# Optimization experiments

Measured on AMD Instinct MI355X. Metric: run time of the kernel, lower is better.

The kernel has to match this reference:

```python
import jax, jax.numpy as jnp
import numpy as np

L, B, E, H, NH = 128, 32, 128, 256, 8
NUM_NODE, ETA = 20000, 100


def setup_inputs() -> dict:
    key = jax.random.key(0)
    ks = jax.random.split(key, 24)
    s = 0.05
    rn = lambda k, sh: jax.random.normal(k, sh, dtype=jnp.float32) * s
    return {
        "node": jax.random.randint(ks[0], (L, B), 0, NUM_NODE + 1),
        "ts": jax.random.normal(ks[1], (L, B, 2), dtype=jnp.float32),
        "seq_lengths": jnp.sort(jax.random.randint(ks[2], (B,), 64, L + 1))[::-1],
        "embed_table": rn(ks[3], (NUM_NODE + 1, E)),
        "Wih0": rn(ks[4], (3 * H, E + 2)), "Whh0": rn(ks[5], (3 * H, H)),
        "bih0": rn(ks[6], (3 * H,)), "bhh0": rn(ks[7], (3 * H,)),
        "Wih1": rn(ks[8], (3 * H, H)), "Whh1": rn(ks[9], (3 * H, H)),
        "bih1": rn(ks[10], (3 * H,)), "bhh1": rn(ks[11], (3 * H,)),
        "Wa0": rn(ks[12], (E, 2 * E)), "ba0": rn(ks[13], (E,)),
        "Wa1": rn(ks[14], (NH, E)), "ba1": rn(ks[15], (NH,)),
        "Wf0": rn(ks[16], (168, H * (NH + 1))), "bf0": rn(ks[17], (168,)),
        "Wf1": rn(ks[18], (ETA, 168)), "bf1": rn(ks[19], (ETA,)),
    }


def gru_layer(x, Wih, Whh, bih, bhh, lengths):
    # x: [L, B, in]; PyTorch GRU cell, with pack/pad semantics:
    # hidden frozen and output zeroed for t >= length (emulates pack_padded_sequence).
    Lx, Bx, _ = x.shape

    def step(h, xs):
        x_t, t = xs
        gi = x_t @ Wih.T + bih          # [B, 3H]
        gh = h @ Whh.T + bhh            # [B, 3H]
        ir, iz, in_ = jnp.split(gi, 3, axis=-1)
        hr, hz, hn = jnp.split(gh, 3, axis=-1)
        r = jax.nn.sigmoid(ir + hr)
        z = jax.nn.sigmoid(iz + hz)
        n = jnp.tanh(in_ + r * hn)
        h_new = (1.0 - z) * n + z * h
        valid = (t < lengths)[:, None]
        h = jnp.where(valid, h_new, h)
        return h, jnp.where(valid, h_new, jnp.zeros_like(h_new))

    h0 = jnp.zeros((Bx, Whh.shape[1]), x.dtype)
    hT, outs = jax.lax.scan(step, h0, (x, jnp.arange(Lx)))
    return outs, hT


def reference(node, ts, seq_lengths, embed_table,
              Wih0, Whh0, bih0, bhh0, Wih1, Whh1, bih1, bhh1,
              Wa0, ba0, Wa1, ba1, Wf0, bf0, Wf1, bf1):
    e = embed_table[node]                          # [L, B, E]
    embeds = jnp.concatenate([e, ts], axis=-1)     # [L, B, E+2]

    # pairwise attention: a[i,j] = e[j], b[i,j] = e[i] (repeat + transpose)
    a = jnp.broadcast_to(e[None], (L, L, B, E))
    b = jnp.broadcast_to(e[:, None], (L, L, B, E))
    pair = jnp.concatenate([a, b], axis=-1)        # [L, L, B, 2E]
    hid = jax.nn.relu(pair @ Wa0.T + ba0)          # [L, L, B, E]
    w = (hid @ Wa1.T + ba1).sum(axis=1)            # [L, B, NH]

    # multiplicative length mask, then softmax over time axis (as in original)
    mask = (jnp.arange(L)[:, None] < seq_lengths[None, :]).astype(w.dtype)[..., None]
    w = jax.nn.softmax(w * mask, axis=0)           # [L, B, NH]

    out0, _ = gru_layer(embeds, Wih0, Whh0, bih0, bhh0, seq_lengths)
    out1, hT = gru_layer(out0, Wih1, Whh1, bih1, bhh1, seq_lengths)  # [L,B,H], [B,H]

    ctx = jnp.einsum('lbh,lbd->bhd', w, out1).reshape(B, NH * H)     # [B, NH*H]
    z = jnp.concatenate([ctx, hT], axis=-1) @ Wf0.T + bf0
    z = jax.nn.selu(z)
    logits = z @ Wf1.T + bf1
    return jax.nn.log_softmax(logits, axis=-1)
```

## Files before the change

kernel.cpp:

```cpp
#include <hip/hip_runtime.h>
#include <hip/hip_bf16.h>

#define LL 128
#define BB 32
#define EE 128
#define HH 256
#define NHH 8
#define G3 768
#define IN0 130
#define ETA 100
#define F1 168
#define CLSIN 2304

typedef _Float16 half_t;
typedef __attribute__((ext_vector_type(2))) _Float16 half2v;
typedef __attribute__((ext_vector_type(8))) _Float16 f16x8;
typedef __attribute__((ext_vector_type(4))) float f32x4;

#if defined(__has_builtin)
#if __has_builtin(__builtin_amdgcn_fdot2)
#define HAVE_FDOT2 1
#endif
#endif

__device__ __forceinline__ float fdot2f(half2v a, half2v b, float c) {
#ifdef HAVE_FDOT2
  return __builtin_amdgcn_fdot2(a, b, c, false);
#else
  return c + (float)a.x * (float)b.x + (float)a.y * (float)b.y;
#endif
}

#define BARRIER_LDS() __asm__ volatile("s_waitcnt lgkmcnt(0)\n\ts_barrier" ::: "memory")

__device__ __forceinline__ float sigmoidf_(float x) { return 1.0f / (1.0f + __expf(-x)); }
__device__ __forceinline__ float tanhf_(float x) { return 1.0f - 2.0f / (__expf(2.0f * x) + 1.0f); }

__global__ void prep_kernel(
    const float* __restrict__ Wa0, const float* __restrict__ Wih0,
    const float* __restrict__ Wih1, const float* __restrict__ Whh0,
    const float* __restrict__ Whh1,
    half_t* __restrict__ Wa0Ta, half_t* __restrict__ Wa0Tb,
    half2v* __restrict__ Wih0T2, half2v* __restrict__ Wih1T2,
    half_t* __restrict__ Whh0h, half_t* __restrict__ Whh1h)
{
  int idx = blockIdx.x * blockDim.x + threadIdx.x;
  const int n1 = 16384, n2 = 16384, n3 = 65 * 768, n4 = 128 * 768, n5 = 196608;
  if (idx < n1) {
    int d = idx >> 7, k = idx & 127;
    Wa0Ta[idx] = (half_t)Wa0[k * 256 + d];
  } else if ((idx -= n1) < n2) {
    int d = idx >> 7, k = idx & 127;
    Wa0Tb[idx] = (half_t)Wa0[k * 256 + 128 + d];
  } else if ((idx -= n2) < n3) {
    int d2 = idx / 768, r = idx % 768;
    half2v w; w.x = (half_t)Wih0[r * IN0 + 2 * d2]; w.y = (half_t)Wih0[r * IN0 + 2 * d2 + 1];
    Wih0T2[idx] = w;
  } else if ((idx -= n3) < n4) {
    int d2 = idx / 768, r = idx % 768;
    half2v w; w.x = (half_t)Wih1[r * HH + 2 * d2]; w.y = (half_t)Wih1[r * HH + 2 * d2 + 1];
    Wih1T2[idx] = w;
  } else if ((idx -= n4) < n5) {
    Whh0h[idx] = (half_t)Whh0[idx];
  } else if ((idx -= n5) < n5) {
    Whh1h[idx] = (half_t)Whh1[idx];
  }
}

__global__ void embed_uv_kernel(
    const int* __restrict__ node,
    const float* __restrict__ table,
    const half_t* __restrict__ Wa0Ta,
    const half_t* __restrict__ Wa0Tb,
    const float* __restrict__ ba0,
    half2v* __restrict__ e_h2,
    float* __restrict__ U,
    float* __restrict__ V)
{
  int lb = blockIdx.x;
  int k = threadIdx.x;
  __shared__ float es[EE];
  int n = node[lb];
  float ev = table[(size_t)n * EE + k];
  es[k] = ev;
  __syncthreads();
  if (k < 64) {
    half2v p; p.x = (half_t)es[2 * k]; p.y = (half_t)es[2 * k + 1];
    e_h2[(size_t)lb * 64 + k] = p;
  }
  float u = 0.f, v = ba0[k];
  #pragma unroll 8
  for (int d = 0; d < EE; ++d) {
    float x = es[d];
    u += (float)Wa0Ta[d * EE + k] * x;
    v += (float)Wa0Tb[d * EE + k] * x;
  }
  U[(size_t)lb * EE + k] = u;
  V[(size_t)lb * EE + k] = v;
}

__global__ __launch_bounds__(128) void attn_w_kernel(
    const float* __restrict__ U, const float* __restrict__ V,
    const float* __restrict__ Wa1,
    const float* __restrict__ ba1,
    float* __restrict__ wpre)
{
  int ig = blockIdx.x >> 5;
  int b = blockIdx.x & 31;
  int i0 = ig * 4;
  int k = threadIdx.x;
  float vk[4];
  #pragma unroll
  for (int ii = 0; ii < 4; ++ii) vk[ii] = V[((size_t)(i0 + ii) * BB + b) * EE + k];
  float wa[NHH], acc[4][NHH];
  #pragma unroll
  for (int h = 0; h < NHH; ++h) wa[h] = Wa1[h * EE + k];
  #pragma unroll
  for (int ii = 0; ii < 4; ++ii)
    #pragma unroll
    for (int h = 0; h < NHH; ++h) acc[ii][h] = 0.f;
  for (int j = 0; j < LL; ++j) {
    float u = U[((size_t)j * BB + b) * EE + k];
    #pragma unroll
    for (int ii = 0; ii < 4; ++ii) {
      float tv = fmaxf(u + vk[ii], 0.f);
      #pragma unroll
      for (int h = 0; h < NHH; ++h) acc[ii][h] += wa[h] * tv;
    }
  }
  __shared__ float part[2][32];
  int wave = k >> 6, lane = k & 63;
  #pragma unroll
  for (int ii = 0; ii < 4; ++ii)
    #pragma unroll
    for (int h = 0; h < NHH; ++h) {
      float a = acc[ii][h];
      #pragma unroll
      for (int off = 32; off > 0; off >>= 1) a += __shfl_xor(a, off, 64);
      if (lane == 0) part[wave][ii * 8 + h] = a;
    }
  __syncthreads();
  if (k < 32) {
    int ii = k >> 3, h = k & 7;
    float w = part[0][k] + part[1][k] + (float)LL * ba1[h];
    wpre[((size_t)(i0 + ii) * BB + b) * NHH + h] = w;
  }
}

__global__ void attn_softmax_kernel(
    const float* __restrict__ wpre, const int* __restrict__ slen,
    float* __restrict__ wsoft)
{
  int b = blockIdx.x >> 3;
  int h = blockIdx.x & 7;
  int l = threadIdx.x;
  int len = slen[b];
  float x = wpre[((size_t)l * BB + b) * NHH + h];
  float xv = (l < len) ? x : 0.f;
  float m = xv;
  #pragma unroll
  for (int off = 32; off > 0; off >>= 1) m = fmaxf(m, __shfl_xor(m, off, 64));
  __shared__ float sm[2], ss[2];
  int wave = l >> 6;
  if ((l & 63) == 0) sm[wave] = m;
  __syncthreads();
  m = fmaxf(sm[0], sm[1]);
  float e = __expf(xv - m);
  float s = e;
  #pragma unroll
  for (int off = 32; off > 0; off >>= 1) s += __shfl_xor(s, off, 64);
  if ((l & 63) == 0) ss[wave] = s;
  __syncthreads();
  s = ss[0] + ss[1];
  wsoft[((size_t)l * BB + b) * NHH + h] = e / s;
}

__global__ __launch_bounds__(256) void gi0_kernel(
    const half2v* __restrict__ e_h2, const float* __restrict__ ts,
    const half2v* __restrict__ W2,
    const float* __restrict__ bih,
    float* __restrict__ gi)
{
  int lb0 = blockIdx.x * 8;
  int tid = threadIdx.x;
  __shared__ half2v xs2[8][66];
  for (int idx = tid; idx < 512; idx += 256) {
    int q = idx >> 6, d2 = idx & 63;
    xs2[q][d2] = e_h2[(size_t)(lb0 + q) * 64 + d2];
  }
  if (tid < 8) {
    half2v t2; t2.x = (half_t)ts[(lb0 + tid) * 2]; t2.y = (half_t)ts[(lb0 + tid) * 2 + 1];
    xs2[tid][64] = t2;
  }
  __syncthreads();
  float acc[8][3];
  #pragma unroll
  for (int q = 0; q < 8; ++q) { acc[q][0] = 0.f; acc[q][1] = 0.f; acc[q][2] = 0.f; }
  for (int d2 = 0; d2 < 65; ++d2) {
    half2v w0 = W2[d2 * 768 + tid];
    half2v w1 = W2[d2 * 768 + 256 + tid];
    half2v w2 = W2[d2 * 768 + 512 + tid];
    #pragma unroll
    for (int q = 0; q < 8; ++q) {
      half2v x = xs2[q][d2];
      acc[q][0] = fdot2f(w0, x, acc[q][0]);
      acc[q][1] = fdot2f(w1, x, acc[q][1]);
      acc[q][2] = fdot2f(w2, x, acc[q][2]);
    }
  }
  float b0 = bih[tid], b1 = bih[256 + tid], b2 = bih[512 + tid];
  #pragma unroll
  for (int q = 0; q < 8; ++q) {
    float* gp = gi + (size_t)(lb0 + q) * G3;
    gp[tid] = acc[q][0] + b0; gp[256 + tid] = acc[q][1] + b1; gp[512 + tid] = acc[q][2] + b2;
  }
}

__global__ __launch_bounds__(256) void gi1_kernel(
    const float* __restrict__ out0,
    const half2v* __restrict__ W2,
    const float* __restrict__ bih,
    float* __restrict__ gi)
{
  int lb0 = blockIdx.x * 8;
  int tid = threadIdx.x;
  __shared__ half2v xs2[8][128];
  for (int idx = tid; idx < 1024; idx += 256) {
    int q = idx >> 7, d2 = idx & 127;
    float2 v = ((const float2*)(out0 + (size_t)(lb0 + q) * HH))[d2];
    half2v x; x.x = (half_t)v.x; x.y = (half_t)v.y;
    xs2[q][d2] = x;
  }
  __syncthreads();
  float acc[8][3];
  #pragma unroll
  for (int q = 0; q < 8; ++q) { acc[q][0] = 0.f; acc[q][1] = 0.f; acc[q][2] = 0.f; }
  for (int d2 = 0; d2 < 128; ++d2) {
    half2v w0 = W2[d2 * 768 + tid];
    half2v w1 = W2[d2 * 768 + 256 + tid];
    half2v w2 = W2[d2 * 768 + 512 + tid];
    #pragma unroll
    for (int q = 0; q < 8; ++q) {
      half2v x = xs2[q][d2];
      acc[q][0] = fdot2f(w0, x, acc[q][0]);
      acc[q][1] = fdot2f(w1, x, acc[q][1]);
      acc[q][2] = fdot2f(w2, x, acc[q][2]);
    }
  }
  float b0 = bih[tid], b1 = bih[256 + tid], b2 = bih[512 + tid];
  #pragma unroll
  for (int q = 0; q < 8; ++q) {
    float* gp = gi + (size_t)(lb0 + q) * G3;
    gp[tid] = acc[q][0] + b0; gp[256 + tid] = acc[q][1] + b1; gp[512 + tid] = acc[q][2] + b2;
  }
}

__global__ __launch_bounds__(512, 2) void gru_scan_kernel(
    const half_t* __restrict__ Whhh,
    const float* __restrict__ bhh,
    const float* __restrict__ gi,
    const int* __restrict__ slen,
    float* __restrict__ out,
    float* __restrict__ hT)
{
  const int b = blockIdx.x;
  const int tid = threadIdx.x;
  const int w = tid >> 6;
  const int lane = tid & 63;
  const int m = lane & 15;
  const int kg = lane >> 4;

  __shared__ __align__(16) half_t hshared[HH];
  __shared__ __align__(16) float gsum[G3];

  f16x8 A[48];
  {
    const half_t* wbase = Whhh + (size_t)(w * 96 + m) * HH + kg * 8;
    #pragma unroll
    for (int tl = 0; tl < 6; ++tl)
      #pragma unroll
      for (int kc = 0; kc < 8; ++kc)
        A[tl * 8 + kc] = *(const f16x8*)(wbase + (size_t)(tl * 16) * HH + kc * 32);
  }

  const int len = slen[b];
  float bhr = 0.f, bhz = 0.f, bhn = 0.f, hold = 0.f;
  if (tid < HH) {
    bhr = bhh[tid]; bhz = bhh[HH + tid]; bhn = bhh[2 * HH + tid];
    hshared[tid] = (half_t)0.f;
  }
  __syncthreads();

  const float* gib = gi + (size_t)b * G3;
  float* outb = out + (size_t)b * HH;

  #pragma unroll 1
  for (int t = 0; t < LL; ++t) {
    float g0 = 0.f, g1 = 0.f, g2 = 0.f;
    if (tid < HH) {
      const float* gp = gib + (size_t)t * (BB * G3);
      g0 = gp[tid]; g1 = gp[HH + tid]; g2 = gp[2 * HH + tid];
    }
    f32x4 C[6];
    #pragma unroll
    for (int tl = 0; tl < 6; ++tl) C[tl] = (f32x4){0.f, 0.f, 0.f, 0.f};
    #pragma unroll
    for (int kc = 0; kc < 8; ++kc) {
      f16x8 bf = *(const f16x8*)&hshared[kc * 32 + kg * 8];
      #pragma unroll
      for (int tl = 0; tl < 6; ++tl)
        C[tl] = __builtin_amdgcn_mfma_f32_16x16x32_f16(A[tl * 8 + kc], bf, C[tl], 0, 0, 0);
    }
    if (m == 0) {
      #pragma unroll
      for (int tl = 0; tl < 6; ++tl)
        *(f32x4*)&gsum[w * 96 + tl * 16 + kg * 4] = C[tl];
    }
    BARRIER_LDS();
    if (tid < HH) {
      float r_ = sigmoidf_(g0 + gsum[tid] + bhr);
      float z_ = sigmoidf_(g1 + gsum[HH + tid] + bhz);
      float n_ = tanhf_(g2 + r_ * (gsum[2 * HH + tid] + bhn));
      float hnew = (1.f - z_) * n_ + z_ * hold;
      bool valid = t < len;
      hold = valid ? hnew : hold;
      hshared[tid] = (half_t)hold;
      outb[(size_t)t * (BB * HH) + tid] = valid ? hnew : 0.f;
    }
    BARRIER_LDS();
  }
  if (tid < HH) hT[(size_t)b * HH + tid] = hold;
}

__global__ void ctx_kernel(
    const float* __restrict__ wsoft, const float* __restrict__ out1,
    float* __restrict__ ctx)
{
  int b = blockIdx.x >> 3, h = blockIdx.x & 7;
  int d = threadIdx.x;
  float acc = 0.f;
  for (int l = 0; l < LL; ++l) {
    float w = wsoft[((size_t)l * BB + b) * NHH + h];
    acc += w * out1[((size_t)l * BB + b) * HH + d];
  }
  ctx[(size_t)b * (NHH * HH) + h * HH + d] = acc;
}

__global__ __launch_bounds__(512) void final_kernel(
    const float* __restrict__ ctx, const float* __restrict__ hT,
    const float* __restrict__ Wf0,
    const float* __restrict__ bf0,
    const float* __restrict__ Wf1,
    const float* __restrict__ bf1,
    float* __restrict__ outp)
{
  int b = blockIdx.x;
  int tid = threadIdx.x;
  int wave = tid >> 6, lane = tid & 63;
  __shared__ float4 xs4[CLSIN / 4];
  __shared__ float zs[F1];
  __shared__ float ls[ETA];
  float* xs = (float*)xs4;
  for (int i = tid; i < NHH * HH; i += 512) xs[i] = ctx[(size_t)b * (NHH * HH) + i];
  if (tid < HH) xs[NHH * HH + tid] = hT[(size_t)b * HH + tid];
  __syncthreads();
  for (int r = wave; r < F1; r += 8) {
    const float4* wp = (const float4*)(Wf0 + (size_t)r * CLSIN);
    float acc = 0.f;
    #pragma unroll
    for (int i = 0; i < CLSIN / 4 / 64; ++i) {
      float4 w = wp[lane + 64 * i];
      float4 x = xs4[lane + 64 * i];
      acc += w.x * x.x + w.y * x.y + w.z * x.z + w.w * x.w;
    }
    #pragma unroll
    for (int off = 32; off > 0; off >>= 1) acc += __shfl_xor(acc, off, 64);
    if (lane == 0) {
      float x = acc + bf0[r];
      const float alpha = 1.6732632423543772f, scale = 1.0507009873554805f;
      zs[r] = scale * (x > 0.f ? x : alpha * (__expf(x) - 1.f));
    }
  }
  __syncthreads();
  for (int r = wave; r < ETA; r += 8) {
    float acc = 0.f;
    for (int k = lane; k < F1; k += 64) acc += Wf1[r * F1 + k] * zs[k];
    #pragma unroll
    for (int off = 32; off > 0; off >>= 1) acc += __shfl_xor(acc, off, 64);
    if (lane == 0) ls[r] = acc + bf1[r];
  }
  __syncthreads();
  if (wave == 0) {
    float v0 = (lane < ETA) ? ls[lane] : -1e30f;
    float v1 = (lane + 64 < ETA) ? ls[lane + 64] : -1e30f;
    float m = fmaxf(v0, v1);
    #pragma unroll
    for (int off = 32; off > 0; off >>= 1) m = fmaxf(m, __shfl_xor(m, off, 64));
    float s = __expf(v0 - m) + __expf(v1 - m);
    #pragma unroll
    for (int off = 32; off > 0; off >>= 1) s += __shfl_xor(s, off, 64);
    float lse = m + __logf(s);
    if (lane < ETA) outp[(size_t)b * ETA + lane] = v0 - lse;
    if (lane + 64 < ETA) outp[(size_t)b * ETA + lane + 64] = v1 - lse;
  }
}

extern "C" void kernel_launch(void* const* d_in, const int* in_sizes, int n_in,
                              void* d_out, int out_size, void* d_ws, size_t ws_size,
                              hipStream_t stream) {
  const int*   node  = (const int*)d_in[0];
  const float* ts    = (const float*)d_in[1];
  const int*   slen  = (const int*)d_in[2];
  const float* table = (const float*)d_in[3];
  const float* Wih0  = (const float*)d_in[4];
  const float* Whh0  = (const float*)d_in[5];
  const float* bih0  = (const float*)d_in[6];
  const float* bhh0  = (const float*)d_in[7];
  const float* Wih1  = (const float*)d_in[8];
  const float* Whh1  = (const float*)d_in[9];
  const float* bih1  = (const float*)d_in[10];
  const float* bhh1  = (const float*)d_in[11];
  const float* Wa0   = (const float*)d_in[12];
  const float* ba0   = (const float*)d_in[13];
  const float* Wa1   = (const float*)d_in[14];
  const float* ba1   = (const float*)d_in[15];
  const float* Wf0   = (const float*)d_in[16];
  const float* bf0   = (const float*)d_in[17];
  const float* Wf1   = (const float*)d_in[18];
  const float* bf1   = (const float*)d_in[19];

  char* ws = (char*)d_ws;
  size_t off = 0;
  auto alloc = [&](size_t n) { void* p = (void*)(ws + off); off += (n + 255) & ~(size_t)255; return p; };

  half2v* e_h2 = (half2v*)alloc((size_t)LL * BB * 64 * 4);
  float* U     = (float*)alloc((size_t)LL * BB * EE * 4);
  float* V     = (float*)alloc((size_t)LL * BB * EE * 4);
  float* gi    = (float*)alloc((size_t)LL * BB * G3 * 4);
  float* out0  = (float*)alloc((size_t)LL * BB * HH * 4);
  float* out1  = (float*)alloc((size_t)LL * BB * HH * 4);
  float* hTb   = (float*)alloc((size_t)BB * HH * 4);
  float* wpre  = (float*)alloc((size_t)LL * BB * NHH * 4);
  float* wsoft = (float*)alloc((size_t)LL * BB * NHH * 4);
  float* ctxb  = (float*)alloc((size_t)BB * NHH * HH * 4);
  half_t* Wa0Ta = (half_t*)alloc((size_t)128 * 128 * 2);
  half_t* Wa0Tb = (half_t*)alloc((size_t)128 * 128 * 2);
  half2v* Wih0T2 = (half2v*)alloc((size_t)65 * 768 * 4);
  half2v* Wih1T2 = (half2v*)alloc((size_t)128 * 768 * 4);
  half_t* Whh0h = (half_t*)alloc((size_t)G3 * HH * 2);
  half_t* Whh1h = (half_t*)alloc((size_t)G3 * HH * 2);
  if (off > ws_size) return;

  const int prep_total = 16384 + 16384 + 65 * 768 + 128 * 768 + 196608 + 196608;
  prep_kernel<<<(prep_total + 255) / 256, 256, 0, stream>>>(
      Wa0, Wih0, Wih1, Whh0, Whh1, Wa0Ta, Wa0Tb, Wih0T2, Wih1T2, Whh0h, Whh1h);
  embed_uv_kernel<<<LL * BB, 128, 0, stream>>>(node, table, Wa0Ta, Wa0Tb, ba0, e_h2, U, V);
  attn_w_kernel<<<(LL / 4) * BB, 128, 0, stream>>>(U, V, Wa1, ba1, wpre);
  attn_softmax_kernel<<<BB * NHH, 128, 0, stream>>>(wpre, slen, wsoft);
  gi0_kernel<<<LL * BB / 8, 256, 0, stream>>>(e_h2, ts, Wih0T2, bih0, gi);
  gru_scan_kernel<<<BB, 512, 0, stream>>>(Whh0h, bhh0, gi, slen, out0, hTb);
  gi1_kernel<<<LL * BB / 8, 256, 0, stream>>>(out0, Wih1T2, bih1, gi);
  gru_scan_kernel<<<BB, 512, 0, stream>>>(Whh1h, bhh1, gi, slen, out1, hTb);
  ctx_kernel<<<BB * NHH, 256, 0, stream>>>(wsoft, out1, ctxb);
  final_kernel<<<BB, 512, 0, stream>>>(ctxb, hTb, Wf0, bf0, Wf1, bf1, (float*)d_out);
}
```

Measured before the change: 638.3 us.

## Remap GRU weight rows so each wave owns gates and double-buffer hidden state

Each wave's MFMA tiles now cover matching r, z and n rows for the same 32 hidden units. The gate nonlinearities are therefore computed directly from the accumulator registers, with no round trip through shared memory. The hidden state is double-buffered in LDS, so each timestep needs one barrier instead of two. The gi loads are vectorized and issued before the MFMAs. The cost is more registers per thread and gate math repeated across lanes that share the same output.

```diff
diff --git a/kernel.cpp b/kernel.cpp
--- a/kernel.cpp
+++ b/kernel.cpp
@@ -14,6 +14,7 @@
 
 typedef _Float16 half_t;
 typedef __attribute__((ext_vector_type(2))) _Float16 half2v;
+typedef __attribute__((ext_vector_type(4))) _Float16 half4v;
 typedef __attribute__((ext_vector_type(8))) _Float16 f16x8;
 typedef __attribute__((ext_vector_type(4))) float f32x4;
 
@@ -270,25 +271,29 @@
   const int m = lane & 15;
   const int kg = lane >> 4;
 
-  __shared__ __align__(16) half_t hshared[HH];
-  __shared__ __align__(16) float gsum[G3];
+  __shared__ __align__(16) half_t hbuf[2][HH];
 
   f16x8 A[48];
-  {
-    const half_t* wbase = Whhh + (size_t)(w * 96 + m) * HH + kg * 8;
-    #pragma unroll
-    for (int tl = 0; tl < 6; ++tl)
-      #pragma unroll
-      for (int kc = 0; kc < 8; ++kc)
-        A[tl * 8 + kc] = *(const f16x8*)(wbase + (size_t)(tl * 16) * HH + kc * 32);
+  #pragma unroll
+  for (int tl = 0; tl < 6; ++tl) {
+    int row = ((tl >> 1) << 8) + w * 32 + ((tl & 1) << 4) + m;
+    const half_t* wbase = Whhh + (size_t)row * HH + kg * 8;
+    #pragma unroll
+    for (int kc = 0; kc < 8; ++kc)
+      A[tl * 8 + kc] = *(const f16x8*)(wbase + kc * 32);
   }
 
   const int len = slen[b];
-  float bhr = 0.f, bhz = 0.f, bhn = 0.f, hold = 0.f;
-  if (tid < HH) {
-    bhr = bhh[tid]; bhz = bhh[HH + tid]; bhn = bhh[2 * HH + tid];
-    hshared[tid] = (half_t)0.f;
-  }
+  const int u0 = w * 32 + kg * 4;
+  float4 br[2], bz[2], bn[2];
+  #pragma unroll
+  for (int j = 0; j < 2; ++j) {
+    br[j] = *(const float4*)(bhh + u0 + j * 16);
+    bz[j] = *(const float4*)(bhh + HH + u0 + j * 16);
+    bn[j] = *(const float4*)(bhh + 2 * HH + u0 + j * 16);
+  }
+  float hold[2][4] = {{0.f, 0.f, 0.f, 0.f}, {0.f, 0.f, 0.f, 0.f}};
+  if (tid < HH) { hbuf[0][tid] = (half_t)0.f; hbuf[1][tid] = (half_t)0.f; }
   __syncthreads();
 
   const float* gib = gi + (size_t)b * G3;
@@ -296,40 +301,64 @@
 
   #pragma unroll 1
   for (int t = 0; t < LL; ++t) {
-    float g0 = 0.f, g1 = 0.f, g2 = 0.f;
-    if (tid < HH) {
-      const float* gp = gib + (size_t)t * (BB * G3);
-      g0 = gp[tid]; g1 = gp[HH + tid]; g2 = gp[2 * HH + tid];
-    }
+    const int p = t & 1;
+    const float* gp = gib + (size_t)t * (BB * G3);
+    float4 gr[2], gz[2], gn[2];
+    #pragma unroll
+    for (int j = 0; j < 2; ++j) {
+      gr[j] = *(const float4*)(gp + u0 + j * 16);
+      gz[j] = *(const float4*)(gp + HH + u0 + j * 16);
+      gn[j] = *(const float4*)(gp + 2 * HH + u0 + j * 16);
+    }
+    f16x8 bf[8];
+    #pragma unroll
+    for (int kc = 0; kc < 8; ++kc)
+      bf[kc] = *(const f16x8*)&hbuf[p][kc * 32 + kg * 8];
     f32x4 C[6];
     #pragma unroll
     for (int tl = 0; tl < 6; ++tl) C[tl] = (f32x4){0.f, 0.f, 0.f, 0.f};
     #pragma unroll
-    for (int kc = 0; kc < 8; ++kc) {
-      f16x8 bf = *(const f16x8*)&hshared[kc * 32 + kg * 8];
+    for (int kc = 0; kc < 8; ++kc)
       #pragma unroll
       for (int tl = 0; tl < 6; ++tl)
-        C[tl] = __builtin_amdgcn_mfma_f32_16x16x32_f16(A[tl * 8 + kc], bf, C[tl], 0, 0, 0);
-    }
-    if (m == 0) {
+        C[tl] = __builtin_amdgcn_mfma_f32_16x16x32_f16(A[tl * 8 + kc], bf[kc], C[tl], 0, 0, 0);
+    bool valid = t < len;
+    #pragma unroll
+    for (int j = 0; j < 2; ++j) {
+      float4 ov;
+      half4v hv;
       #pragma unroll
-      for (int tl = 0; tl < 6; ++tl)
-        *(f32x4*)&gsum[w * 96 + tl * 16 + kg * 4] = C[tl];
+      for (int reg = 0; reg < 4; ++reg) {
+        float grv = (reg == 0 ? gr[j].x : reg == 1 ? gr[j].y : reg == 2 ? gr[j].z : gr[j].w);
+        float gzv = (reg == 0 ? gz[j].x : reg == 1 ? gz[j].y : reg == 2 ? gz[j].z : gz[j].w);
+        float gnv = (reg == 0 ? gn[j].x : reg == 1 ? gn[j].y : reg == 2 ? gn[j].z : gn[j].w);
+        float brv = (reg == 0 ? br[j].x : reg == 1 ? br[j].y : reg == 2 ? br[j].z : br[j].w);
+        float bzv = (reg == 0 ? bz[j].x : reg == 1 ? bz[j].y : reg == 2 ? bz[j].z : bz[j].w);
+        float bnv = (reg == 0 ? bn[j].x : reg == 1 ? bn[j].y : reg == 2 ? bn[j].z : bn[j].w);
+        float r_ = sigmoidf_(grv + C[j][reg] + brv);
+        float z_ = sigmoidf_(gzv + C[2 + j][reg] + bzv);
+        float n_ = tanhf_(gnv + r_ * (C[4 + j][reg] + bnv));
+        float hnew = (1.f - z_) * n_ + z_ * hold[j][reg];
+        hold[j][reg] = valid ? hnew : hold[j][reg];
+        float o = valid ? hnew : 0.f;
+        if (reg == 0) ov.x = o; else if (reg == 1) ov.y = o; else if (reg == 2) ov.z = o; else ov.w = o;
+        hv[reg] = (half_t)hold[j][reg];
+      }
+      if (m == 0) {
+        *(half4v*)&hbuf[p ^ 1][u0 + j * 16] = hv;
+        *(float4*)(outb + (size_t)t * (BB * HH) + u0 + j * 16) = ov;
+      }
     }
     BARRIER_LDS();
-    if (tid < HH) {
-      float r_ = sigmoidf_(g0 + gsum[tid] + bhr);
-      float z_ = sigmoidf_(g1 + gsum[HH + tid] + bhz);
-      float n_ = tanhf_(g2 + r_ * (gsum[2 * HH + tid] + bhn));
-      float hnew = (1.f - z_) * n_ + z_ * hold;
-      bool valid = t < len;
-      hold = valid ? hnew : hold;
-      hshared[tid] = (half_t)hold;
-      outb[(size_t)t * (BB * HH) + tid] = valid ? hnew : 0.f;
-    }
-    BARRIER_LDS();
-  }
-  if (tid < HH) hT[(size_t)b * HH + tid] = hold;
+  }
+  if (m == 0) {
+    #pragma unroll
+    for (int j = 0; j < 2; ++j) {
+      float4 hf;
+      hf.x = hold[j][0]; hf.y = hold[j][1]; hf.z = hold[j][2]; hf.w = hold[j][3];
+      *(float4*)(hT + (size_t)b * HH + u0 + j * 16) = hf;
+    }
+  }
 }
 
 __global__ void ctx_kernel(
```

Result: slower. 1.265 ms (+98.2%).

## Shrink GRU scan to 256 threads with 96 register-held weight fragments and double-buffered hidden state

Applied to the files above, without the earlier changes.

The recurrent scan kernel drops from 512 to 256 threads per block. Each wave now keeps 96 f16x8 weight fragments in registers, with rows laid out so each thread owns one hidden unit across all three gates, which removes the idle half of threads in the gate phase. The hidden state moves to a double buffer in LDS and all eight B fragments are loaded before the MFMA chain. The r and z hidden biases are folded into the precomputed input-gate terms. The risks are very high VGPR pressure from 96 fragments plus 12 accumulators, which could spill, and twice the serial MFMA work per wave.

```diff
diff --git a/kernel.cpp b/kernel.cpp
--- a/kernel.cpp
+++ b/kernel.cpp
@@ -179,6 +179,7 @@
     const half2v* __restrict__ e_h2, const float* __restrict__ ts,
     const half2v* __restrict__ W2,
     const float* __restrict__ bih,
+    const float* __restrict__ bhh,
     float* __restrict__ gi)
 {
   int lb0 = blockIdx.x * 8;
@@ -208,7 +209,9 @@
       acc[q][2] = fdot2f(w2, x, acc[q][2]);
     }
   }
-  float b0 = bih[tid], b1 = bih[256 + tid], b2 = bih[512 + tid];
+  float b0 = bih[tid] + bhh[tid];
+  float b1 = bih[256 + tid] + bhh[256 + tid];
+  float b2 = bih[512 + tid];
   #pragma unroll
   for (int q = 0; q < 8; ++q) {
     float* gp = gi + (size_t)(lb0 + q) * G3;
@@ -220,6 +223,7 @@
     const float* __restrict__ out0,
     const half2v* __restrict__ W2,
     const float* __restrict__ bih,
+    const float* __restrict__ bhh,
     float* __restrict__ gi)
 {
   int lb0 = blockIdx.x * 8;
@@ -247,7 +251,9 @@
       acc[q][2] = fdot2f(w2, x, acc[q][2]);
     }
   }
-  float b0 = bih[tid], b1 = bih[256 + tid], b2 = bih[512 + tid];
+  float b0 = bih[tid] + bhh[tid];
+  float b1 = bih[256 + tid] + bhh[256 + tid];
+  float b2 = bih[512 + tid];
   #pragma unroll
   for (int q = 0; q < 8; ++q) {
     float* gp = gi + (size_t)(lb0 + q) * G3;
@@ -255,7 +261,7 @@
   }
 }
 
-__global__ __launch_bounds__(512, 2) void gru_scan_kernel(
+__global__ __launch_bounds__(256, 1) void gru_scan_kernel(
     const half_t* __restrict__ Whhh,
     const float* __restrict__ bhh,
     const float* __restrict__ gi,
@@ -270,25 +276,26 @@
   const int m = lane & 15;
   const int kg = lane >> 4;
 
-  __shared__ __align__(16) half_t hshared[HH];
+  __shared__ __align__(16) half_t hbuf[2][HH];
   __shared__ __align__(16) float gsum[G3];
 
-  f16x8 A[48];
-  {
-    const half_t* wbase = Whhh + (size_t)(w * 96 + m) * HH + kg * 8;
-    #pragma unroll
-    for (int tl = 0; tl < 6; ++tl)
+  f16x8 A[96];
+  #pragma unroll
+  for (int g = 0; g < 3; ++g)
+    #pragma unroll
+    for (int j = 0; j < 4; ++j) {
+      int row = (g << 8) + (w << 6) + (j << 4) + m;
+      const half_t* wb = Whhh + (size_t)row * HH + kg * 8;
       #pragma unroll
       for (int kc = 0; kc < 8; ++kc)
-        A[tl * 8 + kc] = *(const f16x8*)(wbase + (size_t)(tl * 16) * HH + kc * 32);
-  }
+        A[(g * 4 + j) * 8 + kc] = *(const f16x8*)(wb + kc * 32);
+    }
 
   const int len = slen[b];
-  float bhr = 0.f, bhz = 0.f, bhn = 0.f, hold = 0.f;
-  if (tid < HH) {
-    bhr = bhh[tid]; bhz = bhh[HH + tid]; bhn = bhh[2 * HH + tid];
-    hshared[tid] = (half_t)0.f;
-  }
+  const float bhn = bhh[2 * HH + tid];
+  float hold = 0.f;
+  hbuf[0][tid] = (half_t)0.f;
+  hbuf[1][tid] = (half_t)0.f;
   __syncthreads();
 
   const float* gib = gi + (size_t)b * G3;
@@ -296,40 +303,42 @@
 
   #pragma unroll 1
   for (int t = 0; t < LL; ++t) {
-    float g0 = 0.f, g1 = 0.f, g2 = 0.f;
-    if (tid < HH) {
-      const float* gp = gib + (size_t)t * (BB * G3);
-      g0 = gp[tid]; g1 = gp[HH + tid]; g2 = gp[2 * HH + tid];
-    }
-    f32x4 C[6];
-    #pragma unroll
-    for (int tl = 0; tl < 6; ++tl) C[tl] = (f32x4){0.f, 0.f, 0.f, 0.f};
-    #pragma unroll
-    for (int kc = 0; kc < 8; ++kc) {
-      f16x8 bf = *(const f16x8*)&hshared[kc * 32 + kg * 8];
+    const int p = t & 1;
+    const float* gp = gib + (size_t)t * (BB * G3);
+    float g0 = gp[tid], g1 = gp[HH + tid], g2 = gp[2 * HH + tid];
+    f16x8 bf[8];
+    #pragma unroll
+    for (int kc = 0; kc < 8; ++kc)
+      bf[kc] = *(const f16x8*)&hbuf[p][kc * 32 + kg * 8];
+    f32x4 C[12];
+    #pragma unroll
+    for (int tl = 0; tl < 12; ++tl) C[tl] = (f32x4){0.f, 0.f, 0.f, 0.f};
+    #pragma unroll
+    for (int kc = 0; kc < 8; ++kc)
       #pragma unroll
-      for (int tl = 0; tl < 6; ++tl)
-        C[tl] = __builtin_amdgcn_mfma_f32_16x16x32_f16(A[tl * 8 + kc], bf, C[tl], 0, 0, 0);
-    }
+      for (int tl = 0; tl < 12; ++tl)
+        C[tl] = __builtin_amdgcn_mfma_f32_16x16x32_f16(A[tl * 8 + kc], bf[kc], C[tl], 0, 0, 0);
     if (m == 0) {
       #pragma unroll
-      for (int tl = 0; tl < 6; ++tl)
-        *(f32x4*)&gsum[w * 96 + tl * 16 + kg * 4] = C[tl];
+      for (int g = 0; g < 3; ++g)
+        #pragma unroll
+        for (int j = 0; j < 4; ++j)
+          *(f32x4*)&gsum[(g << 8) + (w << 6) + (j << 4) + (kg << 2)] = C[g * 4 + j];
     }
     BARRIER_LDS();
-    if (tid < HH) {
-      float r_ = sigmoidf_(g0 + gsum[tid] + bhr);
-      float z_ = sigmoidf_(g1 + gsum[HH + tid] + bhz);
+    {
+      float r_ = sigmoidf_(g0 + gsum[tid]);
+      float z_ = sigmoidf_(g1 + gsum[HH + tid]);
       float n_ = tanhf_(g2 + r_ * (gsum[2 * HH + tid] + bhn));
       float hnew = (1.f - z_) * n_ + z_ * hold;
       bool valid = t < len;
       hold = valid ? hnew : hold;
-      hshared[tid] = (half_t)hold;
+      hbuf[p ^ 1][tid] = (half_t)hold;
       outb[(size_t)t * (BB * HH) + tid] = valid ? hnew : 0.f;
     }
     BARRIER_LDS();
   }
-  if (tid < HH) hT[(size_t)b * HH + tid] = hold;
+  hT[(size_t)b * HH + tid] = hold;
 }
 
 __global__ void ctx_kernel(
@@ -457,10 +466,10 @@
   embed_uv_kernel<<<LL * BB, 128, 0, stream>>>(node, table, Wa0Ta, Wa0Tb, ba0, e_h2, U, V);
   attn_w_kernel<<<(LL / 4) * BB, 128, 0, stream>>>(U, V, Wa1, ba1, wpre);
   attn_softmax_kernel<<<BB * NHH, 128, 0, stream>>>(wpre, slen, wsoft);
-  gi0_kernel<<<LL * BB / 8, 256, 0, stream>>>(e_h2, ts, Wih0T2, bih0, gi);
-  gru_scan_kernel<<<BB, 512, 0, stream>>>(Whh0h, bhh0, gi, slen, out0, hTb);
-  gi1_kernel<<<LL * BB / 8, 256, 0, stream>>>(out0, Wih1T2, bih1, gi);
-  gru_scan_kernel<<<BB, 512, 0, stream>>>(Whh1h, bhh1, gi, slen, out1, hTb);
+  gi0_kernel<<<LL * BB / 8, 256, 0, stream>>>(e_h2, ts, Wih0T2, bih0, bhh0, gi);
+  gru_scan_kernel<<<BB, 256, 0, stream>>>(Whh0h, bhh0, gi, slen, out0, hTb);
+  gi1_kernel<<<LL * BB / 8, 256, 0, stream>>>(out0, Wih1T2, bih1, bhh1, gi);
+  gru_scan_kernel<<<BB, 256, 0, stream>>>(Whh1h, bhh1, gi, slen, out1, hTb);
   ctx_kernel<<<BB * NHH, 256, 0, stream>>>(wsoft, out1, ctxb);
   final_kernel<<<BB, 512, 0, stream>>>(ctxb, hTb, Wf0, bf0, Wf1, bf1, (float*)d_out);
 }
```

After: 707.6 us. +10.9%, slower.
